# Kernel tuning notes

Hardware: AMD Instinct MI355X
Metric: run time of the kernel (lower is better)

## Reference

```python
import jax, jax.numpy as jnp
import numpy as np

EQUATION = "bik,bkj->bij"  # matches init_kwargs


def setup_inputs() -> dict:
    key = jax.random.key(0)
    k0, k1 = jax.random.split(key)
    B, I, K, J = 32, 2048, 128, 2048
    input_0 = jax.random.normal(k0, (B, I, K), dtype=jnp.float32)
    input_1 = jax.random.normal(k1, (B, K, J), dtype=jnp.float32)
    return {"input_0": input_0, "input_1": input_1}


def reference(input_0, input_1):
    # Einsum module forward: binary contraction per the stored equation,
    # alpha=1, beta=0 (defaults in EinsumFunction when kwargs is empty).
    return jnp.einsum(EQUATION, input_0, input_1)
```

## Files before the change

### kernel.cpp

```cpp
#include <hip/hip_runtime.h>
#include <hip/hip_bf16.h>
#include <stdint.h>

#define B_DIM 32
#define I_DIM 2048
#define J_DIM 2048
#define K_DIM 128

typedef __attribute__((ext_vector_type(8))) short bf16x8;
typedef __attribute__((ext_vector_type(4))) short short4v;
typedef __attribute__((ext_vector_type(4))) float f32x4;

__device__ inline short f2bf(float f) {
  union { float f; uint32_t u; } v; v.f = f;
  uint32_t u = v.u + 0x7fffu + ((v.u >> 16) & 1u);
  return (short)(u >> 16);
}

__global__ __launch_bounds__(256) void convA_kernel(const float* __restrict__ A,
                                                    short* __restrict__ Ab) {
  const int idx = blockIdx.x * 256 + threadIdx.x;
  const float4* p = reinterpret_cast<const float4*>(A) + (size_t)idx * 2;
  const float4 a = p[0], b = p[1];
  bf16x8 o;
  o[0] = f2bf(a.x); o[1] = f2bf(a.y); o[2] = f2bf(a.z); o[3] = f2bf(a.w);
  o[4] = f2bf(b.x); o[5] = f2bf(b.y); o[6] = f2bf(b.z); o[7] = f2bf(b.w);
  reinterpret_cast<bf16x8*>(Ab)[idx] = o;
}

__global__ __launch_bounds__(256) void transB_kernel(const float* __restrict__ B,
                                                     short* __restrict__ Bt) {
  __shared__ __align__(16) short tile[64 * 128];
  const int t  = threadIdx.x;
  const int j0 = blockIdx.x * 64;
  const int b  = blockIdx.y;
  const float* Bb = B + (size_t)b * K_DIM * J_DIM;
  const int jj = t & 63, kq = t >> 6;
  #pragma unroll
  for (int kr = 0; kr < 32; ++kr) {
    const int k = kr * 4 + kq;
    const float v = Bb[(size_t)k * J_DIM + j0 + jj];
    tile[jj * 128 + (k ^ ((jj & 15) << 3))] = f2bf(v);
  }
  __syncthreads();
  short* Btb = Bt + (size_t)b * J_DIM * K_DIM;
  const int slot = t & 15, jr = t >> 4;
  #pragma unroll
  for (int r2 = 0; r2 < 4; ++r2) {
    const int j  = r2 * 16 + jr;
    const bf16x8 v = *reinterpret_cast<const bf16x8*>(&tile[j * 128 + slot * 8]);
    const int k0 = (slot * 8) ^ ((j & 15) << 3);
    *reinterpret_cast<bf16x8*>(Btb + (size_t)(j0 + j) * K_DIM + k0) = v;
  }
}

#define GLD_LDS16(g, l) __builtin_amdgcn_global_load_lds( \
    (const __attribute__((address_space(1))) uint32_t*)(g), \
    (__attribute__((address_space(3))) uint32_t*)(l), 16, 0, 0)

__global__ __launch_bounds__(256, 2) void gemm_kernel(const short* __restrict__ Ab,
                                                      const short* __restrict__ Bt,
                                                      float* __restrict__ C) {
  __shared__ __align__(16) short As[128 * 128];
  __shared__ __align__(16) short Bs[128 * 128];
  const int t = threadIdx.x;
  const int p = blockIdx.x;
  const int jg = p & 3, it = (p >> 2) & 15, b = p >> 6;

  const int w = t >> 6, wm = w >> 1, wn = w & 1;
  const int lane = t & 63, lr = lane & 15, g = lane >> 4;

  const int srow  = t >> 4;
  const int sbyte = ((t & 15) ^ srow) << 4;
  const char* Asrc  = (const char*)(Ab + ((size_t)b * I_DIM + it * 128 + srow) * K_DIM) + sbyte;
  const char* Bbase = (const char*)(Bt + ((size_t)b * J_DIM + srow) * K_DIM) + sbyte;
  char* Adst = (char*)As + w * 1024;
  char* Bdst = (char*)Bs + w * 1024;

  #pragma unroll
  for (int i = 0; i < 8; ++i) GLD_LDS16(Asrc + i * 4096, Adst + i * 4096);
  {
    const char* Bsrc = Bbase + (size_t)(jg * 4) * 128 * 256;
    #pragma unroll
    for (int i = 0; i < 8; ++i) GLD_LDS16(Bsrc + i * 4096, Bdst + i * 4096);
  }
  asm volatile("s_waitcnt vmcnt(0)" ::: "memory");
  __builtin_amdgcn_sched_barrier(0);
  __builtin_amdgcn_s_barrier();
  __builtin_amdgcn_sched_barrier(0);

  float* Cb = C + (size_t)b * I_DIM * J_DIM;

  #pragma unroll
  for (int q = 0; q < 4; ++q) {
    const int jt = jg * 4 + q;

    f32x4 acc[4][4];
    #pragma unroll
    for (int m = 0; m < 4; ++m)
      #pragma unroll
      for (int n = 0; n < 4; ++n)
        acc[m][n] = (f32x4){0.f, 0.f, 0.f, 0.f};

    #pragma unroll
    for (int kg = 0; kg < 4; ++kg) {
      const int sl = kg * 4 + g;
      bf16x8 af[4], bb[4];
      #pragma unroll
      for (int m = 0; m < 4; ++m) {
        const int R = wm * 64 + m * 16 + lr;
        af[m] = *reinterpret_cast<const bf16x8*>((const char*)As + R * 256 + ((sl ^ lr) << 4));
      }
      #pragma unroll
      for (int n = 0; n < 4; ++n) {
        const int R = wn * 64 + n * 16 + lr;
        bb[n] = *reinterpret_cast<const bf16x8*>((const char*)Bs + R * 256 + ((sl ^ lr) << 4));
      }
      #pragma unroll
      for (int m = 0; m < 4; ++m)
        #pragma unroll
        for (int n = 0; n < 4; ++n)
          acc[m][n] = __builtin_amdgcn_mfma_f32_16x16x32_bf16(af[m], bb[n], acc[m][n], 0, 0, 0);
    }

    __builtin_amdgcn_s_barrier();
    __builtin_amdgcn_sched_barrier(0);

    if (q < 3) {
      const char* Bsrc = Bbase + (size_t)(jt + 1) * 128 * 256;
      #pragma unroll
      for (int i = 0; i < 8; ++i) GLD_LDS16(Bsrc + i * 4096, Bdst + i * 4096);
    }

    const int cbase = jt * 128 + wn * 64 + lr;
    #pragma unroll
    for (int m = 0; m < 4; ++m) {
      const int rbase = it * 128 + wm * 64 + m * 16 + g * 4;
      #pragma unroll
      for (int qq = 0; qq < 4; ++qq) {
        float* crow = Cb + (size_t)(rbase + qq) * J_DIM + cbase;
        #pragma unroll
        for (int n = 0; n < 4; ++n) crow[n * 16] = acc[m][n][qq];
      }
    }

    if (q < 3) {
      asm volatile("s_waitcnt vmcnt(63)" ::: "memory");
      __builtin_amdgcn_sched_barrier(0);
      __builtin_amdgcn_s_barrier();
      __builtin_amdgcn_sched_barrier(0);
    }
  }
}

__device__ inline int swz_fb(int row, int kbyte) {
  return row * 128 + ((kbyte ^ ((row & 15) << 4)) >> 1);
}

__global__ __launch_bounds__(256, 2) void bmm_fallback(const float* __restrict__ A,
                                                       const float* __restrict__ Bm,
                                                       float* __restrict__ C) {
  __shared__ short As[128 * 128];
  __shared__ short Bs[128 * 128];
  const int t  = threadIdx.x;
  const int jt = blockIdx.x, it = blockIdx.y, b = blockIdx.z;
  const float* Abp = A  + (size_t)b * I_DIM * K_DIM;
  const float* Bbp = Bm + (size_t)b * K_DIM * J_DIM;
  {
    const int r0 = t >> 5;
    const int k0 = (t & 31) * 4;
    #pragma unroll 4
    for (int i8 = 0; i8 < 16; ++i8) {
      const int r = i8 * 8 + r0;
      const float4 v = *reinterpret_cast<const float4*>(
          Abp + (size_t)(it * 128 + r) * K_DIM + k0);
      short4v s; s.x = f2bf(v.x); s.y = f2bf(v.y); s.z = f2bf(v.z); s.w = f2bf(v.w);
      *reinterpret_cast<short4v*>(&As[swz_fb(r, 2 * k0)]) = s;
    }
  }
  {
    const int j  = t & 127;
    const int kq = (t >> 7) * 4;
    #pragma unroll 4
    for (int kb = 0; kb < 16; ++kb) {
      const int k0 = kb * 8 + kq;
      const float* p = Bbp + (size_t)k0 * J_DIM + jt * 128 + j;
      const float f0 = p[0], f1 = p[J_DIM], f2 = p[2 * J_DIM], f3 = p[3 * J_DIM];
      short4v s; s.x = f2bf(f0); s.y = f2bf(f1); s.z = f2bf(f2); s.w = f2bf(f3);
      *reinterpret_cast<short4v*>(&Bs[swz_fb(j, 2 * k0)]) = s;
    }
  }
  __syncthreads();
  const int w = t >> 6, wm = w >> 1, wn = w & 1;
  const int lane = t & 63, lr = lane & 15, g = lane >> 4;
  f32x4 acc[4][4];
  #pragma unroll
  for (int m = 0; m < 4; ++m)
    #pragma unroll
    for (int n = 0; n < 4; ++n) acc[m][n] = (f32x4){0.f, 0.f, 0.f, 0.f};
  #pragma unroll
  for (int kk = 0; kk < 4; ++kk) {
    bf16x8 af[4], bfr[4];
    const int kb = kk * 64 + g * 16;
    #pragma unroll
    for (int m = 0; m < 4; ++m) {
      const int r = wm * 64 + m * 16 + lr;
      af[m] = *reinterpret_cast<const bf16x8*>(&As[swz_fb(r, kb)]);
    }
    #pragma unroll
    for (int n = 0; n < 4; ++n) {
      const int r = wn * 64 + n * 16 + lr;
      bfr[n] = *reinterpret_cast<const bf16x8*>(&Bs[swz_fb(r, kb)]);
    }
    #pragma unroll
    for (int m = 0; m < 4; ++m)
      #pragma unroll
      for (int n = 0; n < 4; ++n)
        acc[m][n] = __builtin_amdgcn_mfma_f32_16x16x32_bf16(af[m], bfr[n], acc[m][n], 0, 0, 0);
  }
  float* Cb = C + (size_t)b * I_DIM * J_DIM;
  const int cbase = jt * 128 + wn * 64 + lr;
  #pragma unroll
  for (int m = 0; m < 4; ++m) {
    const int rbase = it * 128 + wm * 64 + m * 16 + g * 4;
    #pragma unroll
    for (int q = 0; q < 4; ++q) {
      float* crow = Cb + (size_t)(rbase + q) * J_DIM + cbase;
      #pragma unroll
      for (int n = 0; n < 4; ++n) crow[n * 16] = acc[m][n][q];
    }
  }
}

extern "C" void kernel_launch(void* const* d_in, const int* in_sizes, int n_in,
                              void* d_out, int out_size, void* d_ws, size_t ws_size,
                              hipStream_t stream) {
  const float* A  = (const float*)d_in[0];
  const float* Bm = (const float*)d_in[1];
  float* C = (float*)d_out;
  const size_t needA = (size_t)B_DIM * I_DIM * K_DIM * sizeof(short);
  const size_t needB = (size_t)B_DIM * K_DIM * J_DIM * sizeof(short);
  if (ws_size >= needA + needB) {
    short* Ab = (short*)d_ws;
    short* Bt = (short*)((char*)d_ws + needA);
    convA_kernel<<<4096, 256, 0, stream>>>(A, Ab);
    transB_kernel<<<dim3(J_DIM / 64, B_DIM), 256, 0, stream>>>(Bm, Bt);
    gemm_kernel<<<2048, 256, 0, stream>>>(Ab, Bt, C);
  } else {
    bmm_fallback<<<dim3(J_DIM / 128, I_DIM / 128, B_DIM), 256, 0, stream>>>(A, Bm, C);
  }
}
```

Baseline: 139.7 us.

## Merge A-convert and B-transpose kernels; give each GEMM block a full J row

The two preprocessing kernels become one launch that branches on block index, which removes a kernel launch and the gap between launches. The GEMM grid shrinks from 2048 to 512 blocks. Each block now keeps its A tile resident and loops over all 16 J tiles, streaming B tiles through LDS, so A is reused more and less A traffic is redundant. The cost is fewer blocks, only 512 at 2 per CU on 256 CUs, which risks tail imbalance and lower latency hiding. The loop is also no longer unrolled.

```diff
diff --git a/kernel.cpp b/kernel.cpp
--- a/kernel.cpp
+++ b/kernel.cpp
@@ -17,23 +17,25 @@
   return (short)(u >> 16);
 }
 
-__global__ __launch_bounds__(256) void convA_kernel(const float* __restrict__ A,
-                                                    short* __restrict__ Ab) {
-  const int idx = blockIdx.x * 256 + threadIdx.x;
-  const float4* p = reinterpret_cast<const float4*>(A) + (size_t)idx * 2;
-  const float4 a = p[0], b = p[1];
-  bf16x8 o;
-  o[0] = f2bf(a.x); o[1] = f2bf(a.y); o[2] = f2bf(a.z); o[3] = f2bf(a.w);
-  o[4] = f2bf(b.x); o[5] = f2bf(b.y); o[6] = f2bf(b.z); o[7] = f2bf(b.w);
-  reinterpret_cast<bf16x8*>(Ab)[idx] = o;
-}
-
-__global__ __launch_bounds__(256) void transB_kernel(const float* __restrict__ B,
-                                                     short* __restrict__ Bt) {
+__global__ __launch_bounds__(256) void prep_kernel(const float* __restrict__ A,
+                                                   const float* __restrict__ B,
+                                                   short* __restrict__ Ab,
+                                                   short* __restrict__ Bt) {
+  const int t = threadIdx.x;
+  if (blockIdx.x < 4096) {
+    const int idx = blockIdx.x * 256 + t;
+    const float4* p = reinterpret_cast<const float4*>(A) + (size_t)idx * 2;
+    const float4 a = p[0], b = p[1];
+    bf16x8 o;
+    o[0] = f2bf(a.x); o[1] = f2bf(a.y); o[2] = f2bf(a.z); o[3] = f2bf(a.w);
+    o[4] = f2bf(b.x); o[5] = f2bf(b.y); o[6] = f2bf(b.z); o[7] = f2bf(b.w);
+    reinterpret_cast<bf16x8*>(Ab)[idx] = o;
+    return;
+  }
   __shared__ __align__(16) short tile[64 * 128];
-  const int t  = threadIdx.x;
-  const int j0 = blockIdx.x * 64;
-  const int b  = blockIdx.y;
+  const int pb = blockIdx.x - 4096;
+  const int j0 = (pb & 31) * 64;
+  const int b  = pb >> 5;
   const float* Bb = B + (size_t)b * K_DIM * J_DIM;
   const int jj = t & 63, kq = t >> 6;
   #pragma unroll
@@ -65,7 +67,7 @@
   __shared__ __align__(16) short Bs[128 * 128];
   const int t = threadIdx.x;
   const int p = blockIdx.x;
-  const int jg = p & 3, it = (p >> 2) & 15, b = p >> 6;
+  const int it = p & 15, b = p >> 4;
 
   const int w = t >> 6, wm = w >> 1, wn = w & 1;
   const int lane = t & 63, lr = lane & 15, g = lane >> 4;
@@ -79,11 +81,8 @@
 
   #pragma unroll
   for (int i = 0; i < 8; ++i) GLD_LDS16(Asrc + i * 4096, Adst + i * 4096);
-  {
-    const char* Bsrc = Bbase + (size_t)(jg * 4) * 128 * 256;
-    #pragma unroll
-    for (int i = 0; i < 8; ++i) GLD_LDS16(Bsrc + i * 4096, Bdst + i * 4096);
-  }
+  #pragma unroll
+  for (int i = 0; i < 8; ++i) GLD_LDS16(Bbase + i * 4096, Bdst + i * 4096);
   asm volatile("s_waitcnt vmcnt(0)" ::: "memory");
   __builtin_amdgcn_sched_barrier(0);
   __builtin_amdgcn_s_barrier();
@@ -91,10 +90,8 @@
 
   float* Cb = C + (size_t)b * I_DIM * J_DIM;
 
-  #pragma unroll
-  for (int q = 0; q < 4; ++q) {
-    const int jt = jg * 4 + q;
-
+  #pragma unroll 1
+  for (int q = 0; q < 16; ++q) {
     f32x4 acc[4][4];
     #pragma unroll
     for (int m = 0; m < 4; ++m)
@@ -126,13 +123,13 @@
     __builtin_amdgcn_s_barrier();
     __builtin_amdgcn_sched_barrier(0);
 
-    if (q < 3) {
-      const char* Bsrc = Bbase + (size_t)(jt + 1) * 128 * 256;
+    if (q < 15) {
+      const char* Bsrc = Bbase + (size_t)(q + 1) * 32768;
       #pragma unroll
       for (int i = 0; i < 8; ++i) GLD_LDS16(Bsrc + i * 4096, Bdst + i * 4096);
     }
 
-    const int cbase = jt * 128 + wn * 64 + lr;
+    const int cbase = q * 128 + wn * 64 + lr;
     #pragma unroll
     for (int m = 0; m < 4; ++m) {
       const int rbase = it * 128 + wm * 64 + m * 16 + g * 4;
@@ -144,7 +141,7 @@
       }
     }
 
-    if (q < 3) {
+    if (q < 15) {
       asm volatile("s_waitcnt vmcnt(63)" ::: "memory");
       __builtin_amdgcn_sched_barrier(0);
       __builtin_amdgcn_s_barrier();
@@ -243,9 +240,8 @@
   if (ws_size >= needA + needB) {
     short* Ab = (short*)d_ws;
     short* Bt = (short*)((char*)d_ws + needA);
-    convA_kernel<<<4096, 256, 0, stream>>>(A, Ab);
-    transB_kernel<<<dim3(J_DIM / 64, B_DIM), 256, 0, stream>>>(Bm, Bt);
-    gemm_kernel<<<2048, 256, 0, stream>>>(Ab, Bt, C);
+    prep_kernel<<<5120, 256, 0, stream>>>(A, Bm, Ab, Bt);
+    gemm_kernel<<<512, 256, 0, stream>>>(Ab, Bt, C);
   } else {
     bmm_fallback<<<dim3(J_DIM / 128, I_DIM / 128, B_DIM), 256, 0, stream>>>(A, Bm, C);
   }
```

After: 152.4 us. 1.09x slower.

## Fuse A fp32-to-bf16 conversion into GEMM prologue and vectorize B transpose loads

Applied to the files above, without the earlier changes.

Drops the separate convA kernel. Each GEMM block now loads its fp32 A panel, converts it to bf16 in registers and writes it swizzled into LDS, which removes the bf16 A write to the workspace and the later re-read. The transB kernel switches to float4 global loads, and the q loop is no longer unrolled, which may cut code size or register pressure. The risk is a slower prologue, since A now takes synchronous register loads instead of async global-to-LDS loads.

```diff
diff --git a/kernel.cpp b/kernel.cpp
--- a/kernel.cpp
+++ b/kernel.cpp
@@ -15,17 +15,6 @@
   union { float f; uint32_t u; } v; v.f = f;
   uint32_t u = v.u + 0x7fffu + ((v.u >> 16) & 1u);
   return (short)(u >> 16);
-}
-
-__global__ __launch_bounds__(256) void convA_kernel(const float* __restrict__ A,
-                                                    short* __restrict__ Ab) {
-  const int idx = blockIdx.x * 256 + threadIdx.x;
-  const float4* p = reinterpret_cast<const float4*>(A) + (size_t)idx * 2;
-  const float4 a = p[0], b = p[1];
-  bf16x8 o;
-  o[0] = f2bf(a.x); o[1] = f2bf(a.y); o[2] = f2bf(a.z); o[3] = f2bf(a.w);
-  o[4] = f2bf(b.x); o[5] = f2bf(b.y); o[6] = f2bf(b.z); o[7] = f2bf(b.w);
-  reinterpret_cast<bf16x8*>(Ab)[idx] = o;
 }
 
 __global__ __launch_bounds__(256) void transB_kernel(const float* __restrict__ B,
@@ -35,12 +24,17 @@
   const int j0 = blockIdx.x * 64;
   const int b  = blockIdx.y;
   const float* Bb = B + (size_t)b * K_DIM * J_DIM;
-  const int jj = t & 63, kq = t >> 6;
-  #pragma unroll
-  for (int kr = 0; kr < 32; ++kr) {
-    const int k = kr * 4 + kq;
-    const float v = Bb[(size_t)k * J_DIM + j0 + jj];
-    tile[jj * 128 + (k ^ ((jj & 15) << 3))] = f2bf(v);
+  const int qj = t & 15;
+  const int k0 = t >> 4;
+  #pragma unroll
+  for (int kp = 0; kp < 8; ++kp) {
+    const int k = kp * 16 + k0;
+    const f32x4 v = *reinterpret_cast<const f32x4*>(Bb + (size_t)k * J_DIM + j0 + 4 * qj);
+    #pragma unroll
+    for (int e = 0; e < 4; ++e) {
+      const int jj = 4 * qj + e;
+      tile[jj * 128 + (k ^ ((jj & 15) << 3))] = f2bf(v[e]);
+    }
   }
   __syncthreads();
   short* Btb = Bt + (size_t)b * J_DIM * K_DIM;
@@ -49,8 +43,8 @@
   for (int r2 = 0; r2 < 4; ++r2) {
     const int j  = r2 * 16 + jr;
     const bf16x8 v = *reinterpret_cast<const bf16x8*>(&tile[j * 128 + slot * 8]);
-    const int k0 = (slot * 8) ^ ((j & 15) << 3);
-    *reinterpret_cast<bf16x8*>(Btb + (size_t)(j0 + j) * K_DIM + k0) = v;
+    const int kk0 = (slot * 8) ^ ((j & 15) << 3);
+    *reinterpret_cast<bf16x8*>(Btb + (size_t)(j0 + j) * K_DIM + kk0) = v;
   }
 }
 
@@ -58,7 +52,7 @@
     (const __attribute__((address_space(1))) uint32_t*)(g), \
     (__attribute__((address_space(3))) uint32_t*)(l), 16, 0, 0)
 
-__global__ __launch_bounds__(256, 2) void gemm_kernel(const short* __restrict__ Ab,
+__global__ __launch_bounds__(256, 2) void gemm_kernel(const float* __restrict__ A,
                                                       const short* __restrict__ Bt,
                                                       float* __restrict__ C) {
   __shared__ __align__(16) short As[128 * 128];
@@ -72,26 +66,36 @@
 
   const int srow  = t >> 4;
   const int sbyte = ((t & 15) ^ srow) << 4;
-  const char* Asrc  = (const char*)(Ab + ((size_t)b * I_DIM + it * 128 + srow) * K_DIM) + sbyte;
   const char* Bbase = (const char*)(Bt + ((size_t)b * J_DIM + srow) * K_DIM) + sbyte;
-  char* Adst = (char*)As + w * 1024;
   char* Bdst = (char*)Bs + w * 1024;
 
-  #pragma unroll
-  for (int i = 0; i < 8; ++i) GLD_LDS16(Asrc + i * 4096, Adst + i * 4096);
-  {
-    const char* Bsrc = Bbase + (size_t)(jg * 4) * 128 * 256;
+  {
+    const char* Bsrc = Bbase + (size_t)(jg * 4) * 32768;
     #pragma unroll
     for (int i = 0; i < 8; ++i) GLD_LDS16(Bsrc + i * 4096, Bdst + i * 4096);
   }
-  asm volatile("s_waitcnt vmcnt(0)" ::: "memory");
+  {
+    const float* Apan = A + ((size_t)b * I_DIM + it * 128) * K_DIM;
+    #pragma unroll
+    for (int j = 0; j < 8; ++j) {
+      const int pp  = t + j * 256;
+      const int row = pp >> 4, g0 = pp & 15;
+      const f32x4 lo = *reinterpret_cast<const f32x4*>(Apan + (size_t)pp * 8);
+      const f32x4 hi = *reinterpret_cast<const f32x4*>(Apan + (size_t)pp * 8 + 4);
+      bf16x8 o;
+      o[0] = f2bf(lo[0]); o[1] = f2bf(lo[1]); o[2] = f2bf(lo[2]); o[3] = f2bf(lo[3]);
+      o[4] = f2bf(hi[0]); o[5] = f2bf(hi[1]); o[6] = f2bf(hi[2]); o[7] = f2bf(hi[3]);
+      *reinterpret_cast<bf16x8*>((char*)As + row * 256 + ((g0 ^ (row & 15)) << 4)) = o;
+    }
+  }
+  asm volatile("s_waitcnt vmcnt(0) lgkmcnt(0)" ::: "memory");
   __builtin_amdgcn_sched_barrier(0);
   __builtin_amdgcn_s_barrier();
   __builtin_amdgcn_sched_barrier(0);
 
   float* Cb = C + (size_t)b * I_DIM * J_DIM;
 
-  #pragma unroll
+  #pragma unroll 1
   for (int q = 0; q < 4; ++q) {
     const int jt = jg * 4 + q;
 
@@ -127,7 +131,7 @@
     __builtin_amdgcn_sched_barrier(0);
 
     if (q < 3) {
-      const char* Bsrc = Bbase + (size_t)(jt + 1) * 128 * 256;
+      const char* Bsrc = Bbase + (size_t)(jt + 1) * 32768;
       #pragma unroll
       for (int i = 0; i < 8; ++i) GLD_LDS16(Bsrc + i * 4096, Bdst + i * 4096);
     }
@@ -238,14 +242,11 @@
   const float* A  = (const float*)d_in[0];
   const float* Bm = (const float*)d_in[1];
   float* C = (float*)d_out;
-  const size_t needA = (size_t)B_DIM * I_DIM * K_DIM * sizeof(short);
   const size_t needB = (size_t)B_DIM * K_DIM * J_DIM * sizeof(short);
-  if (ws_size >= needA + needB) {
-    short* Ab = (short*)d_ws;
-    short* Bt = (short*)((char*)d_ws + needA);
-    convA_kernel<<<4096, 256, 0, stream>>>(A, Ab);
+  if (ws_size >= needB) {
+    short* Bt = (short*)d_ws;
     transB_kernel<<<dim3(J_DIM / 64, B_DIM), 256, 0, stream>>>(Bm, Bt);
-    gemm_kernel<<<2048, 256, 0, stream>>>(Ab, Bt, C);
+    gemm_kernel<<<2048, 256, 0, stream>>>(A, Bt, C);
   } else {
     bmm_fallback<<<dim3(J_DIM / 128, I_DIM / 128, B_DIM), 256, 0, stream>>>(A, Bm, C);
   }
```

Result: faster. 133.1 us (median of 2 runs) (-4.7%).
